# Kernel optimization log

Measured on AMD Instinct MI355X. Metric: run time of the kernel, lower is better.

## Reference

```python
import jax, jax.numpy as jnp
import numpy as np

N = 50000   # total nodes
E = 600000  # total edges
D = 128     # feature dim (node_dim == all gcn_dims)
G = 128     # graphs in batch
LN_EPS = 1e-5


def setup_inputs() -> dict:
    key = jax.random.key(0)
    ks = jax.random.split(key, 16)
    inp = {
        "x": jax.random.normal(ks[0], (N, D), dtype=jnp.float32),
        "edge_index": jax.random.randint(ks[1], (2, E), 0, N),
        "batch": jnp.sort(jax.random.randint(ks[2], (N,), 0, G)),
    }
    for l in range(3):
        inp[f"W{l}"] = jax.random.normal(ks[3 + 4 * l], (D, D), dtype=jnp.float32) / np.float32(np.sqrt(D))
        inp[f"b{l}"] = jnp.zeros((D,), jnp.float32)
        inp[f"g{l}"] = jnp.ones((D,), jnp.float32)   # LayerNorm weight
        inp[f"be{l}"] = jnp.zeros((D,), jnp.float32)  # LayerNorm bias
    return inp


def _gcn_norm(edge_index):
    # PyG GCNConv default: add self-loops, symmetric deg^-1/2 normalization.
    loop = jnp.arange(N, dtype=edge_index.dtype)
    src = jnp.concatenate([edge_index[0], loop])
    dst = jnp.concatenate([edge_index[1], loop])
    deg = jax.ops.segment_sum(jnp.ones(src.shape[0], jnp.float32), dst, num_segments=N)
    dinv = jnp.where(deg > 0, jax.lax.rsqrt(deg), 0.0)
    norm = dinv[src] * dinv[dst]  # [E+N]
    return src, dst, norm


def _block(x, src, dst, norm, W, b, g, be):
    # GCNConv: gather-transform-scatter
    h = x @ W                                   # [N, D]
    msg = h[src] * norm[:, None]                # [E+N, D] gather + scale
    out = jax.ops.segment_sum(msg, dst, num_segments=N) + b
    # LayerNorm
    mu = jnp.mean(out, axis=-1, keepdims=True)
    var = jnp.mean((out - mu) ** 2, axis=-1, keepdims=True)
    out = (out - mu) * jax.lax.rsqrt(var + LN_EPS) * g + be
    # residual (Identity since in==out channels) + SiLU
    return jax.nn.silu(out + x)


def reference(x, edge_index, batch, W0, b0, g0, be0, W1, b1, g1, be1, W2, b2, g2, be2):
    src, dst, norm = _gcn_norm(edge_index)
    params = [(W0, b0, g0, be0), (W1, b1, g1, be1), (W2, b2, g2, be2)]
    for (W, b, g, be) in params:
        x = _block(x, src, dst, norm, W, b, g, be)
    # global mean pool over batch ids
    counts = jax.ops.segment_sum(jnp.ones((N,), jnp.float32), batch, num_segments=G)
    sums = jax.ops.segment_sum(x, batch, num_segments=G)
    return sums / jnp.maximum(counts, 1.0)[:, None]
```

## Files before the change

### kernel.cpp

```cpp
#include <hip/hip_runtime.h>
#include <math.h>

#define DD 128

typedef __attribute__((ext_vector_type(8))) short short8;
typedef __attribute__((ext_vector_type(4))) float f32x4;

__device__ __forceinline__ unsigned short f2b(float f) {
    unsigned int x = __float_as_uint(f);
    return (unsigned short)((x + 0x7FFFu + ((x >> 16) & 1u)) >> 16);
}
__device__ __forceinline__ float b2f(unsigned short u) {
    return __uint_as_float(((unsigned int)u) << 16);
}

__global__ __launch_bounds__(256) void k_setup(const int* __restrict__ dst, int* __restrict__ cnt, int E,
                                               const float* __restrict__ W0, const float* __restrict__ W1,
                                               const float* __restrict__ W2, unsigned short* __restrict__ T0,
                                               unsigned short* __restrict__ T1, unsigned short* __restrict__ T2) {
    int bid = blockIdx.x;
    if (bid < 192) {
        int l = bid >> 6;
        const float* W = (l == 0) ? W0 : (l == 1) ? W1 : W2;
        unsigned short* WT = (l == 0) ? T0 : (l == 1) ? T1 : T2;
        int idx = (bid & 63) * 256 + threadIdx.x;
        int k = idx >> 7, c = idx & 127;
        WT[c * DD + k] = f2b(W[idx]);
    } else {
        int base = ((bid - 192) * 256 + threadIdx.x) * 4;
        if (base + 3 < E) {
            int4 d4 = *(const int4*)(dst + base);
            atomicAdd(&cnt[d4.x], 1);
            atomicAdd(&cnt[d4.y], 1);
            atomicAdd(&cnt[d4.z], 1);
            atomicAdd(&cnt[d4.w], 1);
        } else {
            for (int e = base; e < E; ++e) atomicAdd(&cnt[dst[e]], 1);
        }
    }
}

__global__ __launch_bounds__(256) void k_scan1(const int* __restrict__ cnt, int* __restrict__ part, int N) {
    __shared__ int lds[256];
    int t = threadIdx.x;
    int i = blockIdx.x * 256 + t;
    lds[t] = (i < N) ? cnt[i] : 0;
    __syncthreads();
#pragma unroll
    for (int off = 128; off > 0; off >>= 1) {
        if (t < off) lds[t] += lds[t + off];
        __syncthreads();
    }
    if (t == 0) part[blockIdx.x] = lds[0];
}

__global__ __launch_bounds__(1024) void k_scan2(int* __restrict__ part, int* __restrict__ rowptr,
                                                int nblk, int N) {
    __shared__ int lds[1024];
    int t = threadIdx.x;
    int v = (t < nblk) ? part[t] : 0;
    lds[t] = v;
    __syncthreads();
    for (int off = 1; off < 1024; off <<= 1) {
        int u = (t >= off) ? lds[t - off] : 0;
        __syncthreads();
        lds[t] += u;
        __syncthreads();
    }
    if (t < nblk) part[t] = lds[t] - v;
    if (t == 1023) rowptr[N] = lds[1023];
}

__global__ __launch_bounds__(256) void k_scan3(const int* __restrict__ cnt, const int* __restrict__ part,
                                               int* __restrict__ rowptr, float* __restrict__ dinv, int N) {
    __shared__ int lds[256];
    int t = threadIdx.x;
    int i = blockIdx.x * 256 + t;
    int v = (i < N) ? cnt[i] : 0;
    lds[t] = v;
    __syncthreads();
    for (int off = 1; off < 256; off <<= 1) {
        int u = (t >= off) ? lds[t - off] : 0;
        __syncthreads();
        lds[t] += u;
        __syncthreads();
    }
    if (i < N) {
        rowptr[i] = part[blockIdx.x] + lds[t] - v;
        dinv[i] = rsqrtf((float)v + 1.0f);
    }
}

template <int IN_BF16>
__global__ __launch_bounds__(256) void k_gemm_mfma(const void* __restrict__ Xv,
                                                   const unsigned short* __restrict__ WT,
                                                   const float* __restrict__ dinv,
                                                   unsigned short* __restrict__ H, int N, int gblk,
                                                   const int* __restrict__ src, const int* __restrict__ dst,
                                                   const int* __restrict__ rowptr, int* __restrict__ cursor,
                                                   int* __restrict__ adjS, int E) {
    __shared__ __align__(16) unsigned short sB[DD * DD];
    __shared__ __align__(16) unsigned short sA[DD * DD];
    int tid = threadIdx.x;

    if ((int)blockIdx.x >= gblk) {
        int base = (((int)blockIdx.x - gblk) * 256 + tid) * 4;
        if (base + 3 < E) {
            int4 s4 = *(const int4*)(src + base);
            int4 d4 = *(const int4*)(dst + base);
            int p0 = atomicAdd(&cursor[d4.x], 1);
            int p1 = atomicAdd(&cursor[d4.y], 1);
            int p2 = atomicAdd(&cursor[d4.z], 1);
            int p3 = atomicAdd(&cursor[d4.w], 1);
            adjS[rowptr[d4.x] + p0] = s4.x;
            adjS[rowptr[d4.y] + p1] = s4.y;
            adjS[rowptr[d4.z] + p2] = s4.z;
            adjS[rowptr[d4.w] + p3] = s4.w;
        } else {
            for (int e = base; e < E && e >= 0; ++e) {
                int s = src[e], d = dst[e];
                int pos = atomicAdd(&cursor[d], 1);
                adjS[rowptr[d] + pos] = s;
            }
        }
        return;
    }

    long row0 = (long)blockIdx.x * 128;

#pragma unroll
    for (int i = 0; i < 8; ++i) {
        int q = tid + 256 * i;
        int c = q >> 4, j = q & 15;
        short8 v = *(const short8*)(WT + q * 8);
        int byte = c * 256 + ((j * 16) ^ ((c & 7) << 4));
        *(short8*)((char*)sB + byte) = v;
    }
#pragma unroll
    for (int i = 0; i < 8; ++i) {
        int q = tid + 256 * i;
        int r = q >> 4, j = q & 15;
        short8 v;
        if (IN_BF16) {
#pragma unroll
            for (int z = 0; z < 8; ++z) v[z] = 0;
            if (row0 + r < N) v = *(const short8*)((const unsigned short*)Xv + (row0 + r) * DD + j * 8);
        } else {
            float4 a0 = make_float4(0.f, 0.f, 0.f, 0.f), a1 = a0;
            if (row0 + r < N) {
                const float4* p = (const float4*)((const float*)Xv + (row0 + r) * DD + j * 8);
                a0 = p[0];
                a1 = p[1];
            }
            v[0] = (short)f2b(a0.x); v[1] = (short)f2b(a0.y);
            v[2] = (short)f2b(a0.z); v[3] = (short)f2b(a0.w);
            v[4] = (short)f2b(a1.x); v[5] = (short)f2b(a1.y);
            v[6] = (short)f2b(a1.z); v[7] = (short)f2b(a1.w);
        }
        int byte = r * 256 + ((j * 16) ^ ((r & 7) << 4));
        *(short8*)((char*)sA + byte) = v;
    }
    __syncthreads();

    int w = tid >> 6, l = tid & 63;
    int lr = l & 15, kg = l >> 4;
    int ar0 = w * 32 + lr, ar1 = w * 32 + 16 + lr;
    f32x4 acc0[8] = {}, acc1[8] = {};

#pragma unroll
    for (int step = 0; step < 4; ++step) {
        int koff = step * 64 + kg * 16;
        short8 a0 = *(const short8*)((const char*)sA + ar0 * 256 + (koff ^ ((ar0 & 7) << 4)));
        short8 a1 = *(const short8*)((const char*)sA + ar1 * 256 + (koff ^ ((ar1 & 7) << 4)));
#pragma unroll
        for (int ct = 0; ct < 8; ++ct) {
            int c = ct * 16 + lr;
            short8 bf = *(const short8*)((const char*)sB + c * 256 + (koff ^ ((c & 7) << 4)));
            acc0[ct] = __builtin_amdgcn_mfma_f32_16x16x32_bf16(a0, bf, acc0[ct], 0, 0, 0);
            acc1[ct] = __builtin_amdgcn_mfma_f32_16x16x32_bf16(a1, bf, acc1[ct], 0, 0, 0);
        }
    }

    float dv0[4], dv1[4];
#pragma unroll
    for (int reg = 0; reg < 4; ++reg) {
        long r = row0 + w * 32 + kg * 4 + reg;
        dv0[reg] = (r < N) ? dinv[r] : 0.f;
        dv1[reg] = (r + 16 < N) ? dinv[r + 16] : 0.f;
    }
#pragma unroll
    for (int ct = 0; ct < 8; ++ct) {
#pragma unroll
        for (int reg = 0; reg < 4; ++reg) {
            long r = row0 + w * 32 + kg * 4 + reg;
            if (r < N) H[r * DD + ct * 16 + lr] = f2b(dv0[reg] * acc0[ct][reg]);
            long r2 = r + 16;
            if (r2 < N) H[r2 * DD + ct * 16 + lr] = f2b(dv1[reg] * acc1[ct][reg]);
        }
    }
}

template <int IN_BF16>
__global__ __launch_bounds__(256) void k_agg(const unsigned short* __restrict__ h, const void* __restrict__ xin,
                                             const int* __restrict__ rowptr, const int* __restrict__ adjS,
                                             const float* __restrict__ dinv, const float* __restrict__ b,
                                             const float* __restrict__ g, const float* __restrict__ be,
                                             unsigned int* __restrict__ xout, int N) {
    int row = blockIdx.x * 4 + (threadIdx.x >> 6);
    if (row >= N) return;
    int lane = threadIdx.x & 63;
    const unsigned int* hu = (const unsigned int*)h;

    float dv = dinv[row];
    unsigned int us = hu[(size_t)row * 64 + lane];
    float selfx = b2f((unsigned short)(us & 0xFFFF));
    float selfy = b2f((unsigned short)(us >> 16));
    float2 acc = make_float2(0.f, 0.f);

    int beg = rowptr[row], end = rowptr[row + 1];
    for (int j0 = beg; j0 < end; j0 += 64) {
        int myj = j0 + lane;
        int a = (myj < end) ? adjS[myj] : 0;
        int cnt = min(64, end - j0);
        int cntR = (cnt + 15) & ~15;
        for (int k0 = 0; k0 < cntR; k0 += 16) {
            unsigned int un[16];
#pragma unroll
            for (int u = 0; u < 16; ++u) {
                int s = __shfl(a, k0 + u, 64);
                un[u] = hu[(size_t)s * 64 + lane];
            }
#pragma unroll
            for (int u = 0; u < 16; ++u) {
                float m = (k0 + u < cnt) ? 1.0f : 0.0f;
                acc.x = fmaf(m, b2f((unsigned short)(un[u] & 0xFFFF)), acc.x);
                acc.y = fmaf(m, b2f((unsigned short)(un[u] >> 16)), acc.y);
            }
        }
    }

    float2 bv = ((const float2*)b)[lane];
    float ox = fmaf(dv, selfx + acc.x, bv.x);
    float oy = fmaf(dv, selfy + acc.y, bv.y);

    float ssum = ox + oy;
#pragma unroll
    for (int o = 32; o > 0; o >>= 1) ssum += __shfl_xor(ssum, o, 64);
    float mu = ssum * (1.0f / 128.0f);
    float dx0 = ox - mu, dx1 = oy - mu;
    float vs = dx0 * dx0 + dx1 * dx1;
#pragma unroll
    for (int o = 32; o > 0; o >>= 1) vs += __shfl_xor(vs, o, 64);
    float rstd = rsqrtf(vs * (1.0f / 128.0f) + 1e-5f);

    float2 gv = ((const float2*)g)[lane];
    float2 bev = ((const float2*)be)[lane];
    float2 xv;
    if (IN_BF16) {
        unsigned int xu = ((const unsigned int*)xin)[(size_t)row * 64 + lane];
        xv = make_float2(b2f((unsigned short)(xu & 0xFFFF)), b2f((unsigned short)(xu >> 16)));
    } else {
        xv = ((const float2*)xin)[(size_t)row * 64 + lane];
    }
    float a0 = fmaf(dx0 * rstd, gv.x, bev.x) + xv.x;
    float a1 = fmaf(dx1 * rstd, gv.y, bev.y) + xv.y;
    a0 = a0 / (1.0f + expf(-a0));
    a1 = a1 / (1.0f + expf(-a1));
    xout[(size_t)row * 64 + lane] = ((unsigned int)f2b(a1) << 16) | (unsigned int)f2b(a0);
}

__global__ __launch_bounds__(256) void k_pool2(const unsigned int* __restrict__ x, const int* __restrict__ batch,
                                               float* __restrict__ out, int N) {
    int gi = blockIdx.x;
    int lo = 0, hi = N;
    while (lo < hi) { int m = (lo + hi) >> 1; if (batch[m] < gi) lo = m + 1; else hi = m; }
    int beg = lo;
    lo = beg; hi = N;
    while (lo < hi) { int m = (lo + hi) >> 1; if (batch[m] < gi + 1) lo = m + 1; else hi = m; }
    int end = lo;

    int tid = threadIdx.x;
    int wave = tid >> 6, lane = tid & 63;
    float2 acc = make_float2(0.f, 0.f);
    for (int r = beg + wave; r < end; r += 4) {
        unsigned int u = x[(size_t)r * 64 + lane];
        acc.x += b2f((unsigned short)(u & 0xFFFF));
        acc.y += b2f((unsigned short)(u >> 16));
    }
    __shared__ float part[4][DD];
    ((float2*)part[wave])[lane] = acc;
    __syncthreads();
    if (wave == 0) {
        float sx = 0.f, sy = 0.f;
#pragma unroll
        for (int w = 0; w < 4; ++w) {
            float2 v = ((const float2*)part[w])[lane];
            sx += v.x;
            sy += v.y;
        }
        float inv = 1.0f / fmaxf((float)(end - beg), 1.0f);
        ((float2*)(out + (size_t)gi * DD))[lane] = make_float2(sx * inv, sy * inv);
    }
}

extern "C" void kernel_launch(void* const* d_in, const int* in_sizes, int n_in,
                              void* d_out, int out_size, void* d_ws, size_t ws_size,
                              hipStream_t stream) {
    const float* x = (const float*)d_in[0];
    const int* edge = (const int*)d_in[1];
    const int* batch = (const int*)d_in[2];
    const float* W[3] = {(const float*)d_in[3], (const float*)d_in[7], (const float*)d_in[11]};
    const float* b[3] = {(const float*)d_in[4], (const float*)d_in[8], (const float*)d_in[12]};
    const float* g[3] = {(const float*)d_in[5], (const float*)d_in[9], (const float*)d_in[13]};
    const float* be[3] = {(const float*)d_in[6], (const float*)d_in[10], (const float*)d_in[14]};

    int N = in_sizes[0] / DD;
    int E = in_sizes[1] / 2;
    int G = out_size / DD;
    const int* srcI = edge;
    const int* dstI = edge + E;

    int nblk = (N + 255) / 256;

    char* ws = (char*)d_ws;
    size_t ND = (size_t)N * DD;
    unsigned int* bufX = (unsigned int*)ws;           ws += ND * 2;
    unsigned short* bufH = (unsigned short*)ws;       ws += ND * 2;
    unsigned short* wt[3];
    for (int l = 0; l < 3; ++l) { wt[l] = (unsigned short*)ws; ws += (size_t)DD * DD * 2; }
    float* dinv = (float*)ws;                         ws += (size_t)N * 4;
    int* cnt = (int*)ws;                              ws += (size_t)N * 4;
    int* cursor = (int*)ws;                           ws += (size_t)N * 4;
    int* rowptr = (int*)ws;                           ws += (size_t)(N + 1) * 4;
    int* part = (int*)ws;                             ws += (size_t)nblk * 4;
    int* adjS = (int*)ws;

    hipMemsetAsync(cnt, 0, (size_t)N * 2 * 4, stream);

    int histblk = (E + 1023) / 1024;
    k_setup<<<192 + histblk, 256, 0, stream>>>(dstI, cnt, E, W[0], W[1], W[2], wt[0], wt[1], wt[2]);
    k_scan1<<<nblk, 256, 0, stream>>>(cnt, part, N);
    k_scan2<<<1, 1024, 0, stream>>>(part, rowptr, nblk, N);
    k_scan3<<<nblk, 256, 0, stream>>>(cnt, part, rowptr, dinv, N);

    int gblk = (N + 127) / 128, ablk = (N + 3) / 4;
    int fillblk = (E / 4 + 255) / 256 + 1;
    k_gemm_mfma<0><<<gblk + fillblk, 256, 0, stream>>>(x, wt[0], dinv, bufH, N, gblk,
                                                       srcI, dstI, rowptr, cursor, adjS, E);
    k_agg<0><<<ablk, 256, 0, stream>>>(bufH, x, rowptr, adjS, dinv, b[0], g[0], be[0], bufX, N);
    for (int l = 1; l < 3; ++l) {
        k_gemm_mfma<1><<<gblk, 256, 0, stream>>>(bufX, wt[l], dinv, bufH, N, gblk,
                                                 srcI, dstI, rowptr, cursor, adjS, E);
        k_agg<1><<<ablk, 256, 0, stream>>>(bufH, bufX, rowptr, adjS, dinv, b[l], g[l], be[l], bufX, N);
    }

    k_pool2<<<G, 256, 0, stream>>>(bufX, batch, (float*)d_out, N);
}
```

Baseline: 249.0 us.

## Record atomic ranks in histogram, drop cursor atomics and fold scan2 into scan3

```diff
diff --git a/kernel.cpp b/kernel.cpp
--- a/kernel.cpp
+++ b/kernel.cpp
@@ -14,7 +14,8 @@
     return __uint_as_float(((unsigned int)u) << 16);
 }
 
-__global__ __launch_bounds__(256) void k_setup(const int* __restrict__ dst, int* __restrict__ cnt, int E,
+__global__ __launch_bounds__(256) void k_setup(const int* __restrict__ dst, int* __restrict__ cnt,
+                                               int* __restrict__ rank, int E,
                                                const float* __restrict__ W0, const float* __restrict__ W1,
                                                const float* __restrict__ W2, unsigned short* __restrict__ T0,
                                                unsigned short* __restrict__ T1, unsigned short* __restrict__ T2) {
@@ -30,12 +31,13 @@
         int base = ((bid - 192) * 256 + threadIdx.x) * 4;
         if (base + 3 < E) {
             int4 d4 = *(const int4*)(dst + base);
-            atomicAdd(&cnt[d4.x], 1);
-            atomicAdd(&cnt[d4.y], 1);
-            atomicAdd(&cnt[d4.z], 1);
-            atomicAdd(&cnt[d4.w], 1);
+            int r0 = atomicAdd(&cnt[d4.x], 1);
+            int r1 = atomicAdd(&cnt[d4.y], 1);
+            int r2 = atomicAdd(&cnt[d4.z], 1);
+            int r3 = atomicAdd(&cnt[d4.w], 1);
+            *(int4*)(rank + base) = make_int4(r0, r1, r2, r3);
         } else {
-            for (int e = base; e < E; ++e) atomicAdd(&cnt[dst[e]], 1);
+            for (int e = base; e < E; ++e) rank[e] = atomicAdd(&cnt[dst[e]], 1);
         }
     }
 }
@@ -54,27 +56,22 @@
     if (t == 0) part[blockIdx.x] = lds[0];
 }
 
-__global__ __launch_bounds__(1024) void k_scan2(int* __restrict__ part, int* __restrict__ rowptr,
-                                                int nblk, int N) {
-    __shared__ int lds[1024];
-    int t = threadIdx.x;
-    int v = (t < nblk) ? part[t] : 0;
-    lds[t] = v;
-    __syncthreads();
-    for (int off = 1; off < 1024; off <<= 1) {
-        int u = (t >= off) ? lds[t - off] : 0;
-        __syncthreads();
-        lds[t] += u;
-        __syncthreads();
-    }
-    if (t < nblk) part[t] = lds[t] - v;
-    if (t == 1023) rowptr[N] = lds[1023];
-}
-
 __global__ __launch_bounds__(256) void k_scan3(const int* __restrict__ cnt, const int* __restrict__ part,
-                                               int* __restrict__ rowptr, float* __restrict__ dinv, int N) {
+                                               int* __restrict__ rowptr, float* __restrict__ dinv,
+                                               int N, int nblk) {
+    __shared__ int sp[256];
     __shared__ int lds[256];
     int t = threadIdx.x;
+    sp[t] = (t < nblk) ? part[t] : 0;
+    __syncthreads();
+    for (int off = 1; off < 256; off <<= 1) {
+        int u = (t >= off) ? sp[t - off] : 0;
+        __syncthreads();
+        sp[t] += u;
+        __syncthreads();
+    }
+    int blockOff = (blockIdx.x > 0) ? sp[blockIdx.x - 1] : 0;
+
     int i = blockIdx.x * 256 + t;
     int v = (i < N) ? cnt[i] : 0;
     lds[t] = v;
@@ -86,9 +83,10 @@
         __syncthreads();
     }
     if (i < N) {
-        rowptr[i] = part[blockIdx.x] + lds[t] - v;
+        rowptr[i] = blockOff + lds[t] - v;
         dinv[i] = rsqrtf((float)v + 1.0f);
     }
+    if (blockIdx.x == 0 && t == 0) rowptr[N] = sp[nblk - 1];
 }
 
 template <int IN_BF16>
@@ -97,7 +95,8 @@
                                                    const float* __restrict__ dinv,
                                                    unsigned short* __restrict__ H, int N, int gblk,
                                                    const int* __restrict__ src, const int* __restrict__ dst,
-                                                   const int* __restrict__ rowptr, int* __restrict__ cursor,
+                                                   const int* __restrict__ rank,
+                                                   const int* __restrict__ rowptr,
                                                    int* __restrict__ adjS, int E) {
     __shared__ __align__(16) unsigned short sB[DD * DD];
     __shared__ __align__(16) unsigned short sA[DD * DD];
@@ -108,20 +107,14 @@
         if (base + 3 < E) {
             int4 s4 = *(const int4*)(src + base);
             int4 d4 = *(const int4*)(dst + base);
-            int p0 = atomicAdd(&cursor[d4.x], 1);
-            int p1 = atomicAdd(&cursor[d4.y], 1);
-            int p2 = atomicAdd(&cursor[d4.z], 1);
-            int p3 = atomicAdd(&cursor[d4.w], 1);
-            adjS[rowptr[d4.x] + p0] = s4.x;
-            adjS[rowptr[d4.y] + p1] = s4.y;
-            adjS[rowptr[d4.z] + p2] = s4.z;
-            adjS[rowptr[d4.w] + p3] = s4.w;
+            int4 r4 = *(const int4*)(rank + base);
+            adjS[rowptr[d4.x] + r4.x] = s4.x;
+            adjS[rowptr[d4.y] + r4.y] = s4.y;
+            adjS[rowptr[d4.z] + r4.z] = s4.z;
+            adjS[rowptr[d4.w] + r4.w] = s4.w;
         } else {
-            for (int e = base; e < E && e >= 0; ++e) {
-                int s = src[e], d = dst[e];
-                int pos = atomicAdd(&cursor[d], 1);
-                adjS[rowptr[d] + pos] = s;
-            }
+            for (int e = base; e < E && e >= 0; ++e)
+                adjS[rowptr[dst[e]] + rank[e]] = src[e];
         }
         return;
     }
@@ -330,27 +323,27 @@
     for (int l = 0; l < 3; ++l) { wt[l] = (unsigned short*)ws; ws += (size_t)DD * DD * 2; }
     float* dinv = (float*)ws;                         ws += (size_t)N * 4;
     int* cnt = (int*)ws;                              ws += (size_t)N * 4;
-    int* cursor = (int*)ws;                           ws += (size_t)N * 4;
     int* rowptr = (int*)ws;                           ws += (size_t)(N + 1) * 4;
     int* part = (int*)ws;                             ws += (size_t)nblk * 4;
+    ws = (char*)(((uintptr_t)ws + 15) & ~(uintptr_t)15);
+    int* rank = (int*)ws;                             ws += (size_t)E * 4;
     int* adjS = (int*)ws;
 
-    hipMemsetAsync(cnt, 0, (size_t)N * 2 * 4, stream);
+    hipMemsetAsync(cnt, 0, (size_t)N * 4, stream);
 
     int histblk = (E + 1023) / 1024;
-    k_setup<<<192 + histblk, 256, 0, stream>>>(dstI, cnt, E, W[0], W[1], W[2], wt[0], wt[1], wt[2]);
+    k_setup<<<192 + histblk, 256, 0, stream>>>(dstI, cnt, rank, E, W[0], W[1], W[2], wt[0], wt[1], wt[2]);
     k_scan1<<<nblk, 256, 0, stream>>>(cnt, part, N);
-    k_scan2<<<1, 1024, 0, stream>>>(part, rowptr, nblk, N);
-    k_scan3<<<nblk, 256, 0, stream>>>(cnt, part, rowptr, dinv, N);
+    k_scan3<<<nblk, 256, 0, stream>>>(cnt, part, rowptr, dinv, N, nblk);
 
     int gblk = (N + 127) / 128, ablk = (N + 3) / 4;
     int fillblk = (E / 4 + 255) / 256 + 1;
     k_gemm_mfma<0><<<gblk + fillblk, 256, 0, stream>>>(x, wt[0], dinv, bufH, N, gblk,
-                                                       srcI, dstI, rowptr, cursor, adjS, E);
+                                                       srcI, dstI, rank, rowptr, adjS, E);
     k_agg<0><<<ablk, 256, 0, stream>>>(bufH, x, rowptr, adjS, dinv, b[0], g[0], be[0], bufX, N);
     for (int l = 1; l < 3; ++l) {
         k_gemm_mfma<1><<<gblk, 256, 0, stream>>>(bufX, wt[l], dinv, bufH, N, gblk,
-                                                 srcI, dstI, rowptr, cursor, adjS, E);
+                                                 srcI, dstI, rank, rowptr, adjS, E);
         k_agg<1><<<ablk, 256, 0, stream>>>(bufH, bufX, rowptr, adjS, dinv, b[l], g[l], be[l], bufX, N);
     }
 
```

After: 232.5 us. 6.6% less time.
